# Performance work log

Measured on AMD Instinct MI355X. Metric: run time of the kernel, lower is better.

The kernel has to match this reference:

```python
import jax, jax.numpy as jnp
import numpy as np

B, S, W, D = 64, 512, 400, 1024


def setup_inputs() -> dict:
    key = jax.random.key(0)
    k1, k2, k3 = jax.random.split(key, 3)
    bert_embedding = jax.random.normal(k1, (B, S, D), dtype=jnp.float32)
    # Non-overlapping sorted [st, ed) subword spans per batch row:
    # sort 2*W random boundaries in [0, S) and pair them up.
    bounds = jnp.sort(jax.random.randint(k2, (B, W * 2), 0, S), axis=1)
    x_bert_offset = bounds.reshape(B, W, 2).astype(jnp.int32)
    x_mask = jax.random.randint(k3, (B, W), 0, 2).astype(jnp.int32)
    return {
        "bert_embedding": bert_embedding,
        "x_bert_offset": x_bert_offset,
        "x_mask": x_mask,
    }


def reference(bert_embedding, x_bert_offset, x_mask):
    # bert_embedding: [B, S, D]; x_bert_offset: [B, W, 2]; x_mask: [B, W]
    st = x_bert_offset[..., 0]  # [B, W]
    ed = x_bert_offset[..., 1]  # [B, W]
    pos = jnp.arange(bert_embedding.shape[1])  # [S]
    # span membership mask: [B, W, S]
    span = (pos[None, None, :] >= st[..., None]) & (pos[None, None, :] < ed[..., None])
    span_f = span.astype(bert_embedding.dtype)
    # exact per-word subword sums via dense masked contraction
    sums = jnp.einsum("bws,bsd->bwd", span_f, bert_embedding)  # [B, W, D]
    lens = (ed - st).astype(bert_embedding.dtype)  # [B, W]
    valid = (x_mask != 0) & (ed > st)  # zero rows exactly as torch loop
    mean = sums / jnp.maximum(lens, 1.0)[..., None]
    out = jnp.where(valid[..., None], mean, 0.0)
    return out
```

## Files before the change

### kernel.cpp

```cpp
#include <hip/hip_runtime.h>
#include <hip/hip_bf16.h>

#define BB 64
#define SS 512
#define WW 400
#define DD 1024
#define D4 (DD / 4)

__global__ __launch_bounds__(256) void bert_span_mean(
    const float* __restrict__ emb,
    const int*   __restrict__ offs,
    const int*   __restrict__ mask,
    float*       __restrict__ out)
{
    const int bw = blockIdx.x;
    const int b  = bw / WW;

    const int st = offs[2 * bw];
    const int ed = offs[2 * bw + 1];
    const int m  = mask[bw];

    const int t = threadIdx.x;

    float4 acc = make_float4(0.f, 0.f, 0.f, 0.f);

    const bool valid = (m != 0) && (ed > st);
    if (valid) {
        const float4* src = reinterpret_cast<const float4*>(
            emb + (size_t)b * SS * DD) + t;
        for (int s = st; s < ed; ++s) {
            float4 v = src[(size_t)s * D4];
            acc.x += v.x; acc.y += v.y; acc.z += v.z; acc.w += v.w;
        }
        const float inv = 1.0f / (float)(ed - st);
        acc.x *= inv; acc.y *= inv; acc.z *= inv; acc.w *= inv;
    }

    reinterpret_cast<float4*>(out)[(size_t)bw * D4 + t] = acc;
}

extern "C" void kernel_launch(void* const* d_in, const int* in_sizes, int n_in,
                              void* d_out, int out_size, void* d_ws, size_t ws_size,
                              hipStream_t stream) {
    const float* emb  = (const float*)d_in[0];
    const int*   offs = (const int*)d_in[1];
    const int*   mask = (const int*)d_in[2];
    float*       out  = (float*)d_out;

    const int nblocks = BB * WW;
    bert_span_mean<<<nblocks, 256, 0, stream>>>(emb, offs, mask, out);
}
```

Before: 207.9 us.

## Use persistent grid-stride blocks with prefetched offsets and nontemporal output stores

Replaces one-block-per-word launch with a fixed 2048-block grid that loops over words in a grid-stride fashion. While the current word is processed, the next word's span offsets and mask are prefetched, and the output is written with nontemporal stores so it does not pollute cache. This is meant to cut per-block launch and scheduling overhead and hide the latency of the offset loads. The risk is load imbalance from variable span lengths across a fixed grid, with less freedom for the scheduler.

```diff
diff --git a/kernel.cpp b/kernel.cpp
--- a/kernel.cpp
+++ b/kernel.cpp
@@ -6,37 +6,57 @@
 #define WW 400
 #define DD 1024
 #define D4 (DD / 4)
+#define NWORDS (BB * WW)
 
-__global__ __launch_bounds__(256) void bert_span_mean(
+typedef float vfloat4 __attribute__((ext_vector_type(4)));
+
+__global__ __launch_bounds__(256, 8) void bert_span_mean(
     const float* __restrict__ emb,
     const int*   __restrict__ offs,
     const int*   __restrict__ mask,
     float*       __restrict__ out)
 {
-    const int bw = blockIdx.x;
-    const int b  = bw / WW;
+    const int t = threadIdx.x;
+    const int stride = (int)gridDim.x;
+    const int2* __restrict__ offs2 = reinterpret_cast<const int2*>(offs);
 
-    const int st = offs[2 * bw];
-    const int ed = offs[2 * bw + 1];
-    const int m  = mask[bw];
+    int i = (int)blockIdx.x;
+    int2 cur = offs2[i];
+    int  m   = mask[i];
 
-    const int t = threadIdx.x;
+    while (true) {
+        const int inext = i + stride;
+        int2 nxt = make_int2(0, 0);
+        int  mn  = 0;
+        if (inext < NWORDS) {
+            nxt = offs2[inext];
+            mn  = mask[inext];
+        }
 
-    float4 acc = make_float4(0.f, 0.f, 0.f, 0.f);
+        const int b  = i / WW;
+        const int st = cur.x;
+        const int ed = cur.y;
 
-    const bool valid = (m != 0) && (ed > st);
-    if (valid) {
-        const float4* src = reinterpret_cast<const float4*>(
-            emb + (size_t)b * SS * DD) + t;
-        for (int s = st; s < ed; ++s) {
-            float4 v = src[(size_t)s * D4];
-            acc.x += v.x; acc.y += v.y; acc.z += v.z; acc.w += v.w;
+        vfloat4 acc = (vfloat4)(0.f);
+        if ((m != 0) && (ed > st)) {
+            const vfloat4* src = reinterpret_cast<const vfloat4*>(
+                emb + (size_t)b * SS * DD) + t;
+            for (int s = st; s < ed; ++s) {
+                vfloat4 v = src[(size_t)s * D4];
+                acc += v;
+            }
+            const float inv = 1.0f / (float)(ed - st);
+            acc *= inv;
         }
-        const float inv = 1.0f / (float)(ed - st);
-        acc.x *= inv; acc.y *= inv; acc.z *= inv; acc.w *= inv;
+
+        __builtin_nontemporal_store(acc,
+            reinterpret_cast<vfloat4*>(out) + (size_t)i * D4 + t);
+
+        if (inext >= NWORDS) break;
+        i   = inext;
+        cur = nxt;
+        m   = mn;
     }
-
-    reinterpret_cast<float4*>(out)[(size_t)bw * D4 + t] = acc;
 }
 
 extern "C" void kernel_launch(void* const* d_in, const int* in_sizes, int n_in,
@@ -47,6 +67,5 @@
     const int*   mask = (const int*)d_in[2];
     float*       out  = (float*)d_out;
 
-    const int nblocks = BB * WW;
-    bert_span_mean<<<nblocks, 256, 0, stream>>>(emb, offs, mask, out);
+    bert_span_mean<<<2048, 256, 0, stream>>>(emb, offs, mask, out);
 }
```

Result: no change. 209.4 us (+0.7%).
